# Kernel tuning notes

Hardware: AMD Instinct MI355X
Metric: run time of the kernel (lower is better)

Reference implementation:

```python
import jax, jax.numpy as jnp
import numpy as np
from functools import partial

B = 131072          # training_size (batch)
D_IN = 100          # init_shape
H = 50              # neurons
T = 100             # dimTimes
DT = 0.01           # dt = 1/100
GAMMA = 0.05        # gamma = 1/20
I0 = 0.12


def setup_inputs() -> dict:
    key = jax.random.key(0)
    ks = jax.random.split(key, 7)
    s = lambda fan_in: 1.0 / np.sqrt(fan_in)
    return {
        "x": jax.random.normal(ks[0], (B, D_IN), dtype=jnp.float32),
        "W0": jax.random.uniform(ks[1], (H, D_IN), jnp.float32, -s(D_IN), s(D_IN)),
        "b0": jax.random.uniform(ks[2], (H,), jnp.float32, -s(D_IN), s(D_IN)),
        "W1": jax.random.uniform(ks[3], (H, H), jnp.float32, -s(H), s(H)),
        "b1": jax.random.uniform(ks[4], (H,), jnp.float32, -s(H), s(H)),
        "W2": jax.random.uniform(ks[5], (T - 1, H), jnp.float32, -s(H), s(H)),
        "b2": jax.random.uniform(ks[6], (T - 1,), jnp.float32, -s(H), s(H)),
    }


def reference(x, W0, b0, W1, b1, W2, b2):
    # 3-layer MLP: 100 -> 50 -> 50 -> 99
    h = jax.nn.relu(x @ W0.T + b0)
    h = jax.nn.relu(h @ W1.T + b1)
    out = h @ W2.T + b2                      # [B, T-1] growth rates per step

    # Euler recurrence: I[:,k] = I[:,k-1] + dt*(out[:,k-1]*I*(1-I) - gamma*I)
    i0 = jnp.full((x.shape[0],), I0, dtype=out.dtype)

    def step(I_prev, o_k):
        I_new = I_prev + DT * (o_k * I_prev * (1.0 - I_prev) - GAMMA * I_prev)
        return I_new, I_new

    _, I_rest = jax.lax.scan(step, i0, out.T)   # I_rest: [T-1, B]
    I = jnp.concatenate([i0[:, None], I_rest.T], axis=1)  # [B, T]
    return I
```

## Files before the change

kernel.cpp:

```cpp
#include <hip/hip_runtime.h>
#include <stdint.h>

#define BB      131072
#define TT      100
#define DT_C    0.01f
#define GAMMA_C 0.05f
#define I0_C    0.12f

typedef short bf16x8 __attribute__((ext_vector_type(8)));
typedef float f32x4  __attribute__((ext_vector_type(4)));

#define F0_U16  0
#define F1_U16  (16*512)
#define F2_U16  (24*512)
#define NFRAG_U16 (38*512)

__device__ __forceinline__ uint16_t f2bf(float x) {
    uint32_t u = __builtin_bit_cast(uint32_t, x);
    return (uint16_t)((u + 0x7fffu + ((u >> 16) & 1u)) >> 16);
}

__device__ __forceinline__ uint32_t pk2(float a, float b) {
    uint32_t r;
    asm("v_cvt_pk_bf16_f32 %0, %1, %2" : "=v"(r) : "v"(a), "v"(b));
    return r;
}

__global__ void pack_kernel(const float* __restrict__ W0, const float* __restrict__ b0,
                            const float* __restrict__ W1, const float* __restrict__ b1,
                            const float* __restrict__ W2, const float* __restrict__ b2,
                            uint16_t* __restrict__ wsu)
{
    const int gid = blockIdx.x * blockDim.x + threadIdx.x;
    const int gsz = gridDim.x * blockDim.x;
    for (int idx = gid; idx < NFRAG_U16; idx += gsz) {
        int f = idx >> 9;
        int r = idx & 511;
        int L = r >> 3, j = r & 7;
        int k8 = ((L >> 4) << 3) + j;
        int n16 = L & 15;
        float v = 0.0f;
        if (f < 16) {
            int kc = f >> 2, nt = f & 3;
            int kk = kc * 32 + k8, nn = nt * 16 + n16;
            if (nn < 50) {
                if (kk < 100) v = W0[nn * 100 + kk];
                else if (kk == 100) v = b0[nn];
            }
        } else if (f < 24) {
            int g = f - 16; int kc = g >> 2, nt = g & 3;
            int kk = kc * 32 + k8, nn = nt * 16 + n16;
            if (nn < 50) {
                if (kk < 50) v = W1[nn * 50 + kk];
                else if (kk == 50) v = b1[nn];
            }
        } else {
            int g = f - 24; int kc = g / 7, nt = g % 7;
            int kk = kc * 32 + k8, nn = nt * 16 + n16;
            if (nn < 99) {
                if (kk < 50) v = DT_C * W2[nn * 50 + kk];
                else if (kk == 50) v = DT_C * b2[nn];
            }
        }
        wsu[idx] = f2bf(v);
    }
}

#define SLAB_F 3200

__global__ __launch_bounds__(256, 3) void net_kernel(
    const float* __restrict__ x,
    const void*  __restrict__ wsv,
    float* __restrict__ out)
{
    __shared__ float lds[4 * SLAB_F];
    const int tid  = threadIdx.x;
    const int wave = tid >> 6, lane = tid & 63;
    const int quad = lane >> 4, l15 = lane & 15;
    float* slabF = lds + wave * SLAB_F;
    uint16_t* h0u = (uint16_t*)slabF;
    uint16_t* h1u = (uint16_t*)slabF + 32 * 88;
    const uint16_t* wsu = (const uint16_t*)wsv;

    const int row0 = (blockIdx.x * 4 + wave) * 32;

    bf16x8 a0[2][4];
    #pragma unroll
    for (int h = 0; h < 2; ++h) {
        const float* xrow = x + (size_t)(row0 + h * 16 + l15) * 100;
        #pragma unroll
        for (int kc = 0; kc < 3; ++kc) {
            f32x4 p = *(const f32x4*)(xrow + kc * 32 + quad * 8);
            f32x4 q = *(const f32x4*)(xrow + kc * 32 + quad * 8 + 4);
            union { bf16x8 v; uint32_t u[4]; } t;
            t.u[0] = pk2(p[0], p[1]); t.u[1] = pk2(p[2], p[3]);
            t.u[2] = pk2(q[0], q[1]); t.u[3] = pk2(q[2], q[3]);
            a0[h][kc] = t.v;
        }
        union { bf16x8 v; uint32_t u[4]; } t;
        t.u[0] = t.u[1] = t.u[2] = t.u[3] = 0u;
        if (quad == 0) {
            f32x4 p = *(const f32x4*)(xrow + 96);
            t.u[0] = pk2(p[0], p[1]); t.u[1] = pk2(p[2], p[3]);
            t.u[2] = 0x00003f80u;
        }
        a0[h][3] = t.v;
    }

    f32x4 acc0[2][4];
    #pragma unroll
    for (int h = 0; h < 2; ++h)
        #pragma unroll
        for (int nt = 0; nt < 4; ++nt) acc0[h][nt] = (f32x4){0.f, 0.f, 0.f, 0.f};
    #pragma unroll
    for (int kc = 0; kc < 4; ++kc) {
        #pragma unroll
        for (int nt = 0; nt < 4; ++nt) {
            bf16x8 b = ((const bf16x8*)(wsu + F0_U16 + (kc * 4 + nt) * 512))[lane];
            acc0[0][nt] = __builtin_amdgcn_mfma_f32_16x16x32_bf16(a0[0][kc], b, acc0[0][nt], 0, 0, 0);
            acc0[1][nt] = __builtin_amdgcn_mfma_f32_16x16x32_bf16(a0[1][kc], b, acc0[1][nt], 0, 0, 0);
        }
    }
    const bool is50 = (l15 == 2);
    #pragma unroll
    for (int h = 0; h < 2; ++h) {
        #pragma unroll
        for (int nt = 0; nt < 4; ++nt) {
            const int n = nt * 16 + l15;
            #pragma unroll
            for (int r2 = 0; r2 < 4; r2 += 2) {
                float v0 = fmaxf(acc0[h][nt][r2], 0.0f);
                float v1 = fmaxf(acc0[h][nt][r2 + 1], 0.0f);
                if (nt == 3 && is50) { v0 = 1.0f; v1 = 1.0f; }
                uint32_t p = pk2(v0, v1);
                const int m = h * 16 + quad * 4 + r2;
                h0u[m * 88 + n]       = (uint16_t)p;
                h0u[(m + 1) * 88 + n] = (uint16_t)(p >> 16);
            }
        }
    }

    bf16x8 a1[2][2];
    #pragma unroll
    for (int h = 0; h < 2; ++h)
        #pragma unroll
        for (int kc = 0; kc < 2; ++kc)
            a1[h][kc] = *(const bf16x8*)(h0u + (h * 16 + l15) * 88 + kc * 32 + quad * 8);

    f32x4 acc1[2][4];
    #pragma unroll
    for (int h = 0; h < 2; ++h)
        #pragma unroll
        for (int nt = 0; nt < 4; ++nt) acc1[h][nt] = (f32x4){0.f, 0.f, 0.f, 0.f};
    #pragma unroll
    for (int kc = 0; kc < 2; ++kc) {
        #pragma unroll
        for (int nt = 0; nt < 4; ++nt) {
            bf16x8 b = ((const bf16x8*)(wsu + F1_U16 + (kc * 4 + nt) * 512))[lane];
            acc1[0][nt] = __builtin_amdgcn_mfma_f32_16x16x32_bf16(a1[0][kc], b, acc1[0][nt], 0, 0, 0);
            acc1[1][nt] = __builtin_amdgcn_mfma_f32_16x16x32_bf16(a1[1][kc], b, acc1[1][nt], 0, 0, 0);
        }
    }
    #pragma unroll
    for (int h = 0; h < 2; ++h) {
        #pragma unroll
        for (int nt = 0; nt < 4; ++nt) {
            const int n = nt * 16 + l15;
            #pragma unroll
            for (int r2 = 0; r2 < 4; r2 += 2) {
                float v0 = fmaxf(acc1[h][nt][r2], 0.0f);
                float v1 = fmaxf(acc1[h][nt][r2 + 1], 0.0f);
                if (nt == 3 && is50) { v0 = 1.0f; v1 = 1.0f; }
                uint32_t p = pk2(v0, v1);
                const int m = h * 16 + quad * 4 + r2;
                h1u[m * 88 + n]       = (uint16_t)p;
                h1u[(m + 1) * 88 + n] = (uint16_t)(p >> 16);
            }
        }
    }

    bf16x8 a2[2][2];
    #pragma unroll
    for (int h = 0; h < 2; ++h)
        #pragma unroll
        for (int kc = 0; kc < 2; ++kc)
            a2[h][kc] = *(const bf16x8*)(h1u + (h * 16 + l15) * 88 + kc * 32 + quad * 8);

    {
        f32x4 acc2[2][4];
        #pragma unroll
        for (int h = 0; h < 2; ++h)
            #pragma unroll
            for (int nt = 0; nt < 4; ++nt) acc2[h][nt] = (f32x4){0.f, 0.f, 0.f, 0.f};
        #pragma unroll
        for (int kc = 0; kc < 2; ++kc) {
            #pragma unroll
            for (int nt = 0; nt < 4; ++nt) {
                bf16x8 b = ((const bf16x8*)(wsu + F2_U16 + (kc * 7 + nt) * 512))[lane];
                acc2[0][nt] = __builtin_amdgcn_mfma_f32_16x16x32_bf16(a2[0][kc], b, acc2[0][nt], 0, 0, 0);
                acc2[1][nt] = __builtin_amdgcn_mfma_f32_16x16x32_bf16(a2[1][kc], b, acc2[1][nt], 0, 0, 0);
            }
        }
        #pragma unroll
        for (int h = 0; h < 2; ++h)
            #pragma unroll
            for (int nt = 0; nt < 4; ++nt) {
                const int t = nt * 16 + l15;
                #pragma unroll
                for (int r = 0; r < 4; ++r)
                    slabF[(h * 16 + quad * 4 + r) * 100 + t] = acc2[h][nt][r];
            }
    }
    {
        f32x4 acc2[2][3];
        #pragma unroll
        for (int h = 0; h < 2; ++h)
            #pragma unroll
            for (int nt = 0; nt < 3; ++nt) acc2[h][nt] = (f32x4){0.f, 0.f, 0.f, 0.f};
        #pragma unroll
        for (int kc = 0; kc < 2; ++kc) {
            #pragma unroll
            for (int nt = 0; nt < 3; ++nt) {
                bf16x8 b = ((const bf16x8*)(wsu + F2_U16 + (kc * 7 + (nt + 4)) * 512))[lane];
                acc2[0][nt] = __builtin_amdgcn_mfma_f32_16x16x32_bf16(a2[0][kc], b, acc2[0][nt], 0, 0, 0);
                acc2[1][nt] = __builtin_amdgcn_mfma_f32_16x16x32_bf16(a2[1][kc], b, acc2[1][nt], 0, 0, 0);
            }
        }
        #pragma unroll
        for (int h = 0; h < 2; ++h)
            #pragma unroll
            for (int nt = 0; nt < 3; ++nt) {
                const int t = (nt + 4) * 16 + l15;
                if (nt < 2 || l15 < 3) {
                    #pragma unroll
                    for (int r = 0; r < 4; ++r)
                        slabF[(h * 16 + quad * 4 + r) * 100 + t] = acc2[h][nt][r];
                }
            }
    }

    if (lane < 32) {
        float* orow = slabF + lane * 100;
        const float c = 1.0f - DT_C * GAMMA_C;
        float prev = I0_C;
        #pragma unroll
        for (int ch = 0; ch < 5; ++ch) {
            f32x4 rb[5];
            #pragma unroll
            for (int v = 0; v < 5; ++v)
                rb[v] = *(const f32x4*)(orow + ch * 20 + v * 4);
            float ob[20];
            #pragma unroll
            for (int j = 0; j < 20; ++j) {
                ob[j] = prev;
                if (ch * 20 + j <= 98) {
                    const float op = rb[j >> 2][j & 3];
                    prev = prev * fmaf(-op, prev, c + op);
                }
            }
            #pragma unroll
            for (int v = 0; v < 5; ++v) {
                f32x4 w = { ob[v * 4], ob[v * 4 + 1], ob[v * 4 + 2], ob[v * 4 + 3] };
                *(f32x4*)(orow + ch * 20 + v * 4) = w;
            }
        }
    }

    float* gout = out + (size_t)row0 * 100;
    #pragma unroll
    for (int q = 0; q < 13; ++q) {
        const int i = q * 64 + lane;
        if (i < 800) {
            f32x4 v = *(const f32x4*)(slabF + 4 * i);
            __builtin_nontemporal_store(v, (f32x4*)(gout + 4 * i));
        }
    }
}

extern "C" void kernel_launch(void* const* d_in, const int* in_sizes, int n_in,
                              void* d_out, int out_size, void* d_ws, size_t ws_size,
                              hipStream_t stream) {
    const float* x  = (const float*)d_in[0];
    const float* W0 = (const float*)d_in[1];
    const float* b0 = (const float*)d_in[2];
    const float* W1 = (const float*)d_in[3];
    const float* b1 = (const float*)d_in[4];
    const float* W2 = (const float*)d_in[5];
    const float* b2 = (const float*)d_in[6];
    float* out = (float*)d_out;
    uint16_t* wsu = (uint16_t*)d_ws;

    pack_kernel<<<dim3(80), dim3(256), 0, stream>>>(W0, b0, W1, b1, W2, b2, wsu);
    net_kernel<<<dim3(BB / 128), dim3(256), 0, stream>>>(x, (const void*)wsu, out);
}
```

Measured before the change: 121.4 us.

## Process two row tiles per wave and prefetch the second tile's inputs

Each wave now handles 64 rows as two 32-row tiles, and the grid is halved. The x loads for the second tile are issued before the first tile's MLP and recurrence run, so global load latency overlaps with compute. The cost is 56 extra VGPRs to hold the prefetched floats, which may cut occupancy under the 3-blocks launch bound. There are also half as many blocks to hide latency across CUs.

Result: faster. 117.7 us (median of 2 runs) (-3.0%).

```diff
diff --git a/kernel.cpp b/kernel.cpp
--- a/kernel.cpp
+++ b/kernel.cpp
@@ -68,6 +68,222 @@
 
 #define SLAB_F 3200
 
+__device__ __forceinline__ void load_x_tile(const float* __restrict__ x, int row0,
+                                            int quad, int l15, f32x4 (&xr)[2][7]) {
+    #pragma unroll
+    for (int h = 0; h < 2; ++h) {
+        const float* xrow = x + (size_t)(row0 + h * 16 + l15) * 100;
+        #pragma unroll
+        for (int kc = 0; kc < 3; ++kc) {
+            xr[h][2 * kc]     = *(const f32x4*)(xrow + kc * 32 + quad * 8);
+            xr[h][2 * kc + 1] = *(const f32x4*)(xrow + kc * 32 + quad * 8 + 4);
+        }
+        if (quad == 0) xr[h][6] = *(const f32x4*)(xrow + 96);
+        else           xr[h][6] = (f32x4){0.f, 0.f, 0.f, 0.f};
+    }
+}
+
+__device__ __forceinline__ void convert_x(const f32x4 (&xr)[2][7], int quad,
+                                          bf16x8 (&a0)[2][4]) {
+    #pragma unroll
+    for (int h = 0; h < 2; ++h) {
+        #pragma unroll
+        for (int kc = 0; kc < 3; ++kc) {
+            f32x4 p = xr[h][2 * kc], q = xr[h][2 * kc + 1];
+            union { bf16x8 v; uint32_t u[4]; } t;
+            t.u[0] = pk2(p[0], p[1]); t.u[1] = pk2(p[2], p[3]);
+            t.u[2] = pk2(q[0], q[1]); t.u[3] = pk2(q[2], q[3]);
+            a0[h][kc] = t.v;
+        }
+        union { bf16x8 v; uint32_t u[4]; } t;
+        t.u[0] = t.u[1] = t.u[2] = t.u[3] = 0u;
+        if (quad == 0) {
+            f32x4 p = xr[h][6];
+            t.u[0] = pk2(p[0], p[1]); t.u[1] = pk2(p[2], p[3]);
+            t.u[2] = 0x00003f80u;
+        }
+        a0[h][3] = t.v;
+    }
+}
+
+__device__ __forceinline__ void process_tile(const bf16x8 (&a0)[2][4],
+                                             const uint16_t* __restrict__ wsu,
+                                             float* __restrict__ slabF,
+                                             float* __restrict__ out, int row0,
+                                             int lane, int quad, int l15) {
+    uint16_t* h0u = (uint16_t*)slabF;
+    uint16_t* h1u = (uint16_t*)slabF + 32 * 88;
+    const bool is50 = (l15 == 2);
+
+    f32x4 acc0[2][4];
+    #pragma unroll
+    for (int h = 0; h < 2; ++h)
+        #pragma unroll
+        for (int nt = 0; nt < 4; ++nt) acc0[h][nt] = (f32x4){0.f, 0.f, 0.f, 0.f};
+    #pragma unroll
+    for (int kc = 0; kc < 4; ++kc) {
+        #pragma unroll
+        for (int nt = 0; nt < 4; ++nt) {
+            bf16x8 b = ((const bf16x8*)(wsu + F0_U16 + (kc * 4 + nt) * 512))[lane];
+            acc0[0][nt] = __builtin_amdgcn_mfma_f32_16x16x32_bf16(a0[0][kc], b, acc0[0][nt], 0, 0, 0);
+            acc0[1][nt] = __builtin_amdgcn_mfma_f32_16x16x32_bf16(a0[1][kc], b, acc0[1][nt], 0, 0, 0);
+        }
+    }
+    #pragma unroll
+    for (int h = 0; h < 2; ++h) {
+        #pragma unroll
+        for (int nt = 0; nt < 4; ++nt) {
+            const int n = nt * 16 + l15;
+            #pragma unroll
+            for (int r2 = 0; r2 < 4; r2 += 2) {
+                float v0 = fmaxf(acc0[h][nt][r2], 0.0f);
+                float v1 = fmaxf(acc0[h][nt][r2 + 1], 0.0f);
+                if (nt == 3 && is50) { v0 = 1.0f; v1 = 1.0f; }
+                uint32_t p = pk2(v0, v1);
+                const int m = h * 16 + quad * 4 + r2;
+                h0u[m * 88 + n]       = (uint16_t)p;
+                h0u[(m + 1) * 88 + n] = (uint16_t)(p >> 16);
+            }
+        }
+    }
+
+    bf16x8 a1[2][2];
+    #pragma unroll
+    for (int h = 0; h < 2; ++h)
+        #pragma unroll
+        for (int kc = 0; kc < 2; ++kc)
+            a1[h][kc] = *(const bf16x8*)(h0u + (h * 16 + l15) * 88 + kc * 32 + quad * 8);
+
+    f32x4 acc1[2][4];
+    #pragma unroll
+    for (int h = 0; h < 2; ++h)
+        #pragma unroll
+        for (int nt = 0; nt < 4; ++nt) acc1[h][nt] = (f32x4){0.f, 0.f, 0.f, 0.f};
+    #pragma unroll
+    for (int kc = 0; kc < 2; ++kc) {
+        #pragma unroll
+        for (int nt = 0; nt < 4; ++nt) {
+            bf16x8 b = ((const bf16x8*)(wsu + F1_U16 + (kc * 4 + nt) * 512))[lane];
+            acc1[0][nt] = __builtin_amdgcn_mfma_f32_16x16x32_bf16(a1[0][kc], b, acc1[0][nt], 0, 0, 0);
+            acc1[1][nt] = __builtin_amdgcn_mfma_f32_16x16x32_bf16(a1[1][kc], b, acc1[1][nt], 0, 0, 0);
+        }
+    }
+    #pragma unroll
+    for (int h = 0; h < 2; ++h) {
+        #pragma unroll
+        for (int nt = 0; nt < 4; ++nt) {
+            const int n = nt * 16 + l15;
+            #pragma unroll
+            for (int r2 = 0; r2 < 4; r2 += 2) {
+                float v0 = fmaxf(acc1[h][nt][r2], 0.0f);
+                float v1 = fmaxf(acc1[h][nt][r2 + 1], 0.0f);
+                if (nt == 3 && is50) { v0 = 1.0f; v1 = 1.0f; }
+                uint32_t p = pk2(v0, v1);
+                const int m = h * 16 + quad * 4 + r2;
+                h1u[m * 88 + n]       = (uint16_t)p;
+                h1u[(m + 1) * 88 + n] = (uint16_t)(p >> 16);
+            }
+        }
+    }
+
+    bf16x8 a2[2][2];
+    #pragma unroll
+    for (int h = 0; h < 2; ++h)
+        #pragma unroll
+        for (int kc = 0; kc < 2; ++kc)
+            a2[h][kc] = *(const bf16x8*)(h1u + (h * 16 + l15) * 88 + kc * 32 + quad * 8);
+
+    {
+        f32x4 acc2[2][4];
+        #pragma unroll
+        for (int h = 0; h < 2; ++h)
+            #pragma unroll
+            for (int nt = 0; nt < 4; ++nt) acc2[h][nt] = (f32x4){0.f, 0.f, 0.f, 0.f};
+        #pragma unroll
+        for (int kc = 0; kc < 2; ++kc) {
+            #pragma unroll
+            for (int nt = 0; nt < 4; ++nt) {
+                bf16x8 b = ((const bf16x8*)(wsu + F2_U16 + (kc * 7 + nt) * 512))[lane];
+                acc2[0][nt] = __builtin_amdgcn_mfma_f32_16x16x32_bf16(a2[0][kc], b, acc2[0][nt], 0, 0, 0);
+                acc2[1][nt] = __builtin_amdgcn_mfma_f32_16x16x32_bf16(a2[1][kc], b, acc2[1][nt], 0, 0, 0);
+            }
+        }
+        #pragma unroll
+        for (int h = 0; h < 2; ++h)
+            #pragma unroll
+            for (int nt = 0; nt < 4; ++nt) {
+                const int t = nt * 16 + l15;
+                #pragma unroll
+                for (int r = 0; r < 4; ++r)
+                    slabF[(h * 16 + quad * 4 + r) * 100 + t] = acc2[h][nt][r];
+            }
+    }
+    {
+        f32x4 acc2[2][3];
+        #pragma unroll
+        for (int h = 0; h < 2; ++h)
+            #pragma unroll
+            for (int nt = 0; nt < 3; ++nt) acc2[h][nt] = (f32x4){0.f, 0.f, 0.f, 0.f};
+        #pragma unroll
+        for (int kc = 0; kc < 2; ++kc) {
+            #pragma unroll
+            for (int nt = 0; nt < 3; ++nt) {
+                bf16x8 b = ((const bf16x8*)(wsu + F2_U16 + (kc * 7 + (nt + 4)) * 512))[lane];
+                acc2[0][nt] = __builtin_amdgcn_mfma_f32_16x16x32_bf16(a2[0][kc], b, acc2[0][nt], 0, 0, 0);
+                acc2[1][nt] = __builtin_amdgcn_mfma_f32_16x16x32_bf16(a2[1][kc], b, acc2[1][nt], 0, 0, 0);
+            }
+        }
+        #pragma unroll
+        for (int h = 0; h < 2; ++h)
+            #pragma unroll
+            for (int nt = 0; nt < 3; ++nt) {
+                const int t = (nt + 4) * 16 + l15;
+                if (nt < 2 || l15 < 3) {
+                    #pragma unroll
+                    for (int r = 0; r < 4; ++r)
+                        slabF[(h * 16 + quad * 4 + r) * 100 + t] = acc2[h][nt][r];
+                }
+            }
+    }
+
+    if (lane < 32) {
+        float* orow = slabF + lane * 100;
+        const float c = 1.0f - DT_C * GAMMA_C;
+        float prev = I0_C;
+        #pragma unroll
+        for (int ch = 0; ch < 5; ++ch) {
+            f32x4 rb[5];
+            #pragma unroll
+            for (int v = 0; v < 5; ++v)
+                rb[v] = *(const f32x4*)(orow + ch * 20 + v * 4);
+            float ob[20];
+            #pragma unroll
+            for (int j = 0; j < 20; ++j) {
+                ob[j] = prev;
+                if (ch * 20 + j <= 98) {
+                    const float op = rb[j >> 2][j & 3];
+                    prev = prev * fmaf(-op, prev, c + op);
+                }
+            }
+            #pragma unroll
+            for (int v = 0; v < 5; ++v) {
+                f32x4 w = { ob[v * 4], ob[v * 4 + 1], ob[v * 4 + 2], ob[v * 4 + 3] };
+                *(f32x4*)(orow + ch * 20 + v * 4) = w;
+            }
+        }
+    }
+
+    float* gout = out + (size_t)row0 * 100;
+    #pragma unroll
+    for (int q = 0; q < 13; ++q) {
+        const int i = q * 64 + lane;
+        if (i < 800) {
+            f32x4 v = *(const f32x4*)(slabF + 4 * i);
+            __builtin_nontemporal_store(v, (f32x4*)(gout + 4 * i));
+        }
+    }
+}
+
 __global__ __launch_bounds__(256, 3) void net_kernel(
     const float* __restrict__ x,
     const void*  __restrict__ wsv,
@@ -78,203 +294,19 @@
     const int wave = tid >> 6, lane = tid & 63;
     const int quad = lane >> 4, l15 = lane & 15;
     float* slabF = lds + wave * SLAB_F;
-    uint16_t* h0u = (uint16_t*)slabF;
-    uint16_t* h1u = (uint16_t*)slabF + 32 * 88;
     const uint16_t* wsu = (const uint16_t*)wsv;
 
-    const int row0 = (blockIdx.x * 4 + wave) * 32;
-
-    bf16x8 a0[2][4];
-    #pragma unroll
-    for (int h = 0; h < 2; ++h) {
-        const float* xrow = x + (size_t)(row0 + h * 16 + l15) * 100;
-        #pragma unroll
-        for (int kc = 0; kc < 3; ++kc) {
-            f32x4 p = *(const f32x4*)(xrow + kc * 32 + quad * 8);
-            f32x4 q = *(const f32x4*)(xrow + kc * 32 + quad * 8 + 4);
-            union { bf16x8 v; uint32_t u[4]; } t;
-            t.u[0] = pk2(p[0], p[1]); t.u[1] = pk2(p[2], p[3]);
-            t.u[2] = pk2(q[0], q[1]); t.u[3] = pk2(q[2], q[3]);
-            a0[h][kc] = t.v;
-        }
-        union { bf16x8 v; uint32_t u[4]; } t;
-        t.u[0] = t.u[1] = t.u[2] = t.u[3] = 0u;
-        if (quad == 0) {
-            f32x4 p = *(const f32x4*)(xrow + 96);
-            t.u[0] = pk2(p[0], p[1]); t.u[1] = pk2(p[2], p[3]);
-            t.u[2] = 0x00003f80u;
-        }
-        a0[h][3] = t.v;
-    }
-
-    f32x4 acc0[2][4];
-    #pragma unroll
-    for (int h = 0; h < 2; ++h)
-        #pragma unroll
-        for (int nt = 0; nt < 4; ++nt) acc0[h][nt] = (f32x4){0.f, 0.f, 0.f, 0.f};
-    #pragma unroll
-    for (int kc = 0; kc < 4; ++kc) {
-        #pragma unroll
-        for (int nt = 0; nt < 4; ++nt) {
-            bf16x8 b = ((const bf16x8*)(wsu + F0_U16 + (kc * 4 + nt) * 512))[lane];
-            acc0[0][nt] = __builtin_amdgcn_mfma_f32_16x16x32_bf16(a0[0][kc], b, acc0[0][nt], 0, 0, 0);
-            acc0[1][nt] = __builtin_amdgcn_mfma_f32_16x16x32_bf16(a0[1][kc], b, acc0[1][nt], 0, 0, 0);
-        }
-    }
-    const bool is50 = (l15 == 2);
-    #pragma unroll
-    for (int h = 0; h < 2; ++h) {
-        #pragma unroll
-        for (int nt = 0; nt < 4; ++nt) {
-            const int n = nt * 16 + l15;
-            #pragma unroll
-            for (int r2 = 0; r2 < 4; r2 += 2) {
-                float v0 = fmaxf(acc0[h][nt][r2], 0.0f);
-                float v1 = fmaxf(acc0[h][nt][r2 + 1], 0.0f);
-                if (nt == 3 && is50) { v0 = 1.0f; v1 = 1.0f; }
-                uint32_t p = pk2(v0, v1);
-                const int m = h * 16 + quad * 4 + r2;
-                h0u[m * 88 + n]       = (uint16_t)p;
-                h0u[(m + 1) * 88 + n] = (uint16_t)(p >> 16);
-            }
-        }
-    }
-
-    bf16x8 a1[2][2];
-    #pragma unroll
-    for (int h = 0; h < 2; ++h)
-        #pragma unroll
-        for (int kc = 0; kc < 2; ++kc)
-            a1[h][kc] = *(const bf16x8*)(h0u + (h * 16 + l15) * 88 + kc * 32 + quad * 8);
-
-    f32x4 acc1[2][4];
-    #pragma unroll
-    for (int h = 0; h < 2; ++h)
-        #pragma unroll
-        for (int nt = 0; nt < 4; ++nt) acc1[h][nt] = (f32x4){0.f, 0.f, 0.f, 0.f};
-    #pragma unroll
-    for (int kc = 0; kc < 2; ++kc) {
-        #pragma unroll
-        for (int nt = 0; nt < 4; ++nt) {
-            bf16x8 b = ((const bf16x8*)(wsu + F1_U16 + (kc * 4 + nt) * 512))[lane];
-            acc1[0][nt] = __builtin_amdgcn_mfma_f32_16x16x32_bf16(a1[0][kc], b, acc1[0][nt], 0, 0, 0);
-            acc1[1][nt] = __builtin_amdgcn_mfma_f32_16x16x32_bf16(a1[1][kc], b, acc1[1][nt], 0, 0, 0);
-        }
-    }
-    #pragma unroll
-    for (int h = 0; h < 2; ++h) {
-        #pragma unroll
-        for (int nt = 0; nt < 4; ++nt) {
-            const int n = nt * 16 + l15;
-            #pragma unroll
-            for (int r2 = 0; r2 < 4; r2 += 2) {
-                float v0 = fmaxf(acc1[h][nt][r2], 0.0f);
-                float v1 = fmaxf(acc1[h][nt][r2 + 1], 0.0f);
-                if (nt == 3 && is50) { v0 = 1.0f; v1 = 1.0f; }
-                uint32_t p = pk2(v0, v1);
-                const int m = h * 16 + quad * 4 + r2;
-                h1u[m * 88 + n]       = (uint16_t)p;
-                h1u[(m + 1) * 88 + n] = (uint16_t)(p >> 16);
-            }
-        }
-    }
-
-    bf16x8 a2[2][2];
-    #pragma unroll
-    for (int h = 0; h < 2; ++h)
-        #pragma unroll
-        for (int kc = 0; kc < 2; ++kc)
-            a2[h][kc] = *(const bf16x8*)(h1u + (h * 16 + l15) * 88 + kc * 32 + quad * 8);
-
-    {
-        f32x4 acc2[2][4];
-        #pragma unroll
-        for (int h = 0; h < 2; ++h)
-            #pragma unroll
-            for (int nt = 0; nt < 4; ++nt) acc2[h][nt] = (f32x4){0.f, 0.f, 0.f, 0.f};
-        #pragma unroll
-        for (int kc = 0; kc < 2; ++kc) {
-            #pragma unroll
-            for (int nt = 0; nt < 4; ++nt) {
-                bf16x8 b = ((const bf16x8*)(wsu + F2_U16 + (kc * 7 + nt) * 512))[lane];
-                acc2[0][nt] = __builtin_amdgcn_mfma_f32_16x16x32_bf16(a2[0][kc], b, acc2[0][nt], 0, 0, 0);
-                acc2[1][nt] = __builtin_amdgcn_mfma_f32_16x16x32_bf16(a2[1][kc], b, acc2[1][nt], 0, 0, 0);
-            }
-        }
-        #pragma unroll
-        for (int h = 0; h < 2; ++h)
-            #pragma unroll
-            for (int nt = 0; nt < 4; ++nt) {
-                const int t = nt * 16 + l15;
-                #pragma unroll
-                for (int r = 0; r < 4; ++r)
-                    slabF[(h * 16 + quad * 4 + r) * 100 + t] = acc2[h][nt][r];
-            }
-    }
-    {
-        f32x4 acc2[2][3];
-        #pragma unroll
-        for (int h = 0; h < 2; ++h)
-            #pragma unroll
-            for (int nt = 0; nt < 3; ++nt) acc2[h][nt] = (f32x4){0.f, 0.f, 0.f, 0.f};
-        #pragma unroll
-        for (int kc = 0; kc < 2; ++kc) {
-            #pragma unroll
-            for (int nt = 0; nt < 3; ++nt) {
-                bf16x8 b = ((const bf16x8*)(wsu + F2_U16 + (kc * 7 + (nt + 4)) * 512))[lane];
-                acc2[0][nt] = __builtin_amdgcn_mfma_f32_16x16x32_bf16(a2[0][kc], b, acc2[0][nt], 0, 0, 0);
-                acc2[1][nt] = __builtin_amdgcn_mfma_f32_16x16x32_bf16(a2[1][kc], b, acc2[1][nt], 0, 0, 0);
-            }
-        }
-        #pragma unroll
-        for (int h = 0; h < 2; ++h)
-            #pragma unroll
-            for (int nt = 0; nt < 3; ++nt) {
-                const int t = (nt + 4) * 16 + l15;
-                if (nt < 2 || l15 < 3) {
-                    #pragma unroll
-                    for (int r = 0; r < 4; ++r)
-                        slabF[(h * 16 + quad * 4 + r) * 100 + t] = acc2[h][nt][r];
-                }
-            }
-    }
-
-    if (lane < 32) {
-        float* orow = slabF + lane * 100;
-        const float c = 1.0f - DT_C * GAMMA_C;
-        float prev = I0_C;
-        #pragma unroll
-        for (int ch = 0; ch < 5; ++ch) {
-            f32x4 rb[5];
-            #pragma unroll
-            for (int v = 0; v < 5; ++v)
-                rb[v] = *(const f32x4*)(orow + ch * 20 + v * 4);
-            float ob[20];
-            #pragma unroll
-            for (int j = 0; j < 20; ++j) {
-                ob[j] = prev;
-                if (ch * 20 + j <= 98) {
-                    const float op = rb[j >> 2][j & 3];
-                    prev = prev * fmaf(-op, prev, c + op);
-                }
-            }
-            #pragma unroll
-            for (int v = 0; v < 5; ++v) {
-                f32x4 w = { ob[v * 4], ob[v * 4 + 1], ob[v * 4 + 2], ob[v * 4 + 3] };
-                *(f32x4*)(orow + ch * 20 + v * 4) = w;
-            }
-        }
-    }
-
-    float* gout = out + (size_t)row0 * 100;
-    #pragma unroll
-    for (int q = 0; q < 13; ++q) {
-        const int i = q * 64 + lane;
-        if (i < 800) {
-            f32x4 v = *(const f32x4*)(slabF + 4 * i);
-            __builtin_nontemporal_store(v, (f32x4*)(gout + 4 * i));
-        }
-    }
+    const int base = (blockIdx.x * 4 + wave) * 64;
+
+    f32x4 xr[2][7];
+    bf16x8 a0t0[2][4], a0t1[2][4];
+
+    load_x_tile(x, base, quad, l15, xr);
+    convert_x(xr, quad, a0t0);
+    load_x_tile(x, base + 32, quad, l15, xr);
+    process_tile(a0t0, wsu, slabF, out, base, lane, quad, l15);
+    convert_x(xr, quad, a0t1);
+    process_tile(a0t1, wsu, slabF, out, base + 32, lane, quad, l15);
 }
 
 extern "C" void kernel_launch(void* const* d_in, const int* in_sizes, int n_in,
@@ -291,5 +323,5 @@
     uint16_t* wsu = (uint16_t*)d_ws;
 
     pack_kernel<<<dim3(80), dim3(256), 0, stream>>>(W0, b0, W1, b1, W2, b2, wsu);
-    net_kernel<<<dim3(BB / 128), dim3(256), 0, stream>>>(x, (const void*)wsu, out);
-}
+    net_kernel<<<dim3(BB / 256), dim3(256), 0, stream>>>(x, (const void*)wsu, out);
+}
```
